# Optimization experiments

Hardware: AMD Instinct MI355X
Metric: run time of the kernel (lower is better)

## Reference

```python
import jax, jax.numpy as jnp
import numpy as np

B, S, D, H, DH = 2, 2048, 1024, 16, 64
R_ATTN, R_OUT, I, R_FC1, R_FC2 = 32, 512, 4096, 512, 512
LN_EPS = 1e-5


def _layernorm(x, g, b):
    mu = jnp.mean(x, axis=-1, keepdims=True)
    var = jnp.mean(jnp.square(x - mu), axis=-1, keepdims=True)
    return (x - mu) * jax.lax.rsqrt(var + LN_EPS) * g + b


def setup_inputs() -> dict:
    key = jax.random.key(0)
    ks = jax.random.split(key, 16)
    std = 0.02
    return {
        'hidden_states': jax.random.normal(ks[0], (B, S, D), jnp.float32),
        'ln1_g': jnp.ones((D,), jnp.float32),
        'ln1_b': jnp.zeros((D,), jnp.float32),
        'ln2_g': jnp.ones((D,), jnp.float32),
        'ln2_b': jnp.zeros((D,), jnp.float32),
        'q_U': jax.random.normal(ks[1], (D, H, R_ATTN), jnp.float32) * std,
        'q_V': jax.random.normal(ks[2], (H, R_ATTN, DH), jnp.float32) * std,
        'q_b': jnp.zeros((H, DH), jnp.float32),
        'k_U': jax.random.normal(ks[3], (D, H, R_ATTN), jnp.float32) * std,
        'k_V': jax.random.normal(ks[4], (H, R_ATTN, DH), jnp.float32) * std,
        'k_b': jnp.zeros((H, DH), jnp.float32),
        'v_U': jax.random.normal(ks[5], (D, H, R_ATTN), jnp.float32) * std,
        'v_V': jax.random.normal(ks[6], (H, R_ATTN, DH), jnp.float32) * std,
        'v_b': jnp.zeros((H, DH), jnp.float32),
        'out_U': jax.random.normal(ks[7], (D, R_OUT), jnp.float32) * std,
        'out_V': jax.random.normal(ks[8], (R_OUT, D), jnp.float32) * std,
        'out_b': jnp.zeros((D,), jnp.float32),
        'fc1_U': jax.random.normal(ks[9], (D, R_FC1), jnp.float32) * std,
        'fc1_V': jax.random.normal(ks[10], (R_FC1, I), jnp.float32) * std,
        'fc1_b': jnp.zeros((I,), jnp.float32),
        'fc2_U': jax.random.normal(ks[11], (I, R_FC2), jnp.float32) * std,
        'fc2_V': jax.random.normal(ks[12], (R_FC2, D), jnp.float32) * std,
        'fc2_b': jnp.zeros((D,), jnp.float32),
    }


def reference(hidden_states, ln1_g, ln1_b, ln2_g, ln2_b,
              q_U, q_V, q_b, k_U, k_V, k_b, v_U, v_V, v_b,
              out_U, out_V, out_b, fc1_U, fc1_V, fc1_b, fc2_U, fc2_V, fc2_b):
    Bx, Sx, Dx = hidden_states.shape
    scale = 1.0 / np.sqrt(DH).astype(np.float32)
    x = _layernorm(hidden_states, ln1_g, ln1_b)
    # low-rank per-head QKV: [B,S,D]x[D,H,r]x[H,r,dh] -> [B,H,S,dh]
    Q = jnp.einsum('bsd,dhr,hre->bhse', x, q_U, q_V) + q_b[None, :, None, :]
    K = jnp.einsum('bsd,dhr,hre->bhse', x, k_U, k_V) + k_b[None, :, None, :]
    V = jnp.einsum('bsd,dhr,hre->bhse', x, v_U, v_V) + v_b[None, :, None, :]
    scores = jnp.einsum('bhse,bhte->bhst', Q, K) * scale  # [B,H,S,S]
    causal = jnp.tril(jnp.ones((Sx, Sx), bool))
    neg_inf = jnp.finfo(scores.dtype).min
    scores = jnp.where(causal, scores, neg_inf)
    probs = jax.nn.softmax(scores, axis=-1)
    Y = jnp.einsum('bhst,bhte->bhse', probs, V)
    Y = Y.transpose(0, 2, 1, 3).reshape(Bx, Sx, Dx)  # merge heads
    Y = (Y @ out_U) @ out_V + out_b
    h = hidden_states + Y
    z = _layernorm(h, ln2_g, ln2_b)
    h1 = jax.nn.gelu((z @ fc1_U) @ fc1_V + fc1_b, approximate=False)
    h2 = (h1 @ fc2_U) @ fc2_V + fc2_b
    return h + h2
```

## Files before the change

### kernel.cpp

```cpp
#include <hip/hip_runtime.h>
#include <cstdint>
#include <cstddef>


#define NTOK 4096
#define DM   1024
#define SEQ  2048

typedef __attribute__((ext_vector_type(8))) __bf16 bf16x8;
typedef __attribute__((ext_vector_type(4))) __bf16 bf16x4;
typedef __attribute__((ext_vector_type(4))) float  f32x4;

__device__ __forceinline__ f32x4 mfma16(bf16x8 a, bf16x8 b, f32x4 c) {
  return __builtin_amdgcn_mfma_f32_16x16x32_bf16(a, b, c, 0, 0, 0);
}

__device__ __forceinline__ void gload16(const __bf16* g, __bf16* l) {
  __builtin_amdgcn_global_load_lds(
      (const __attribute__((address_space(1))) void*)g,
      (__attribute__((address_space(3))) void*)l, 16, 0, 0);
}

__global__ __launch_bounds__(256) void transpose_k(const float* __restrict__ in,
                                                   __bf16* __restrict__ out,
                                                   int R, int C) {
  __shared__ __bf16 t[32][33];
  int tx = threadIdx.x & 31, ty = threadIdx.x >> 5;
  int r0 = blockIdx.y * 32, c0 = blockIdx.x * 32;
#pragma unroll
  for (int i = 0; i < 32; i += 8)
    t[ty + i][tx] = (__bf16)in[(size_t)(r0 + ty + i) * C + c0 + tx];
  __syncthreads();
#pragma unroll
  for (int i = 0; i < 32; i += 8)
    out[(size_t)(c0 + ty + i) * R + r0 + tx] = t[tx][ty + i];
}

__global__ __launch_bounds__(256) void trans_v(const __bf16* __restrict__ qkv,
                                               __bf16* __restrict__ VT) {
  __shared__ __bf16 t[32][33];
  int tx = threadIdx.x & 31, ty = threadIdx.x >> 5;
  int bh = blockIdx.z, b = bh >> 4, h = bh & 15;
  int k0 = blockIdx.x * 32, d0 = blockIdx.y * 32;
#pragma unroll
  for (int i = 0; i < 32; i += 8)
    t[ty + i][tx] = qkv[(size_t)(b * SEQ + k0 + ty + i) * 3072 + 2048 + h * 64 + d0 + tx];
  __syncthreads();
#pragma unroll
  for (int i = 0; i < 32; i += 8)
    VT[(size_t)(bh * 64 + d0 + ty + i) * SEQ + k0 + tx] = t[tx][ty + i];
}

__global__ __launch_bounds__(256) void combine_uv(const float* __restrict__ qU,
                                                  const float* __restrict__ qV,
                                                  const float* __restrict__ kU,
                                                  const float* __restrict__ kV,
                                                  const float* __restrict__ vU,
                                                  const float* __restrict__ vV,
                                                  __bf16* __restrict__ WT) {
  __shared__ float sV[2048];
  int tid = threadIdx.x;
  int blk = blockIdx.x;
  int sel = blk >> 7;
  int rem = blk & 127;
  int h = rem >> 3, dc = rem & 7;
  int d0 = dc << 7;
  const float* U = sel == 0 ? qU : (sel == 1 ? kU : vU);
  const float* V = sel == 0 ? qV : (sel == 1 ? kV : vV);
  for (int i = tid; i < 2048; i += 256) sV[i] = V[h * 2048 + i];
  int d = d0 + (tid & 127);
  int eh = tid >> 7;
  const float* up = U + (size_t)d * 512 + h * 32;
  float u[32];
#pragma unroll
  for (int i = 0; i < 8; i++)
    *(float4*)&u[i * 4] = *(const float4*)(up + i * 4);
  __syncthreads();
  int e0 = eh * 32;
#pragma unroll
  for (int eg = 0; eg < 8; eg++) {
    float ax = 0.f, ay = 0.f, az = 0.f, aw = 0.f;
#pragma unroll
    for (int r = 0; r < 32; r++) {
      float4 v4 = *(const float4*)&sV[r * 64 + e0 + eg * 4];
      ax += u[r] * v4.x; ay += u[r] * v4.y;
      az += u[r] * v4.z; aw += u[r] * v4.w;
    }
    size_t prow = (size_t)(sel * 1024 + h * 64 + e0 + eg * 4) * 1024 + d;
    WT[prow]        = (__bf16)ax;
    WT[prow + 1024] = (__bf16)ay;
    WT[prow + 2048] = (__bf16)az;
    WT[prow + 3072] = (__bf16)aw;
  }
}

__global__ void concat3(const float* a, const float* b, const float* c, float* o) {
  int i = blockIdx.x * 256 + threadIdx.x;
  o[i] = (i < 1024) ? a[i] : (i < 2048 ? b[i - 1024] : c[i - 2048]);
}

__global__ __launch_bounds__(256) void cast_k(const float* __restrict__ in,
                                              __bf16* __restrict__ out, int n) {
  int i = blockIdx.x * 256 + threadIdx.x;
  if (i < n) out[i] = (__bf16)in[i];
}

template <int TWO>
__global__ __launch_bounds__(256) void ln_k(const float* __restrict__ x,
                                            const __bf16* __restrict__ x2,
                                            const float* __restrict__ g,
                                            const float* __restrict__ b,
                                            __bf16* __restrict__ out) {
  int row = blockIdx.x, tid = threadIdx.x;
  const float* xr = x + (size_t)row * DM;
  float v[4], s = 0.f, ss = 0.f;
#pragma unroll
  for (int i = 0; i < 4; i++) {
    int c = i * 256 + tid;
    v[i] = xr[c];
    if (TWO) v[i] += (float)x2[(size_t)row * DM + c];
    s += v[i]; ss += v[i] * v[i];
  }
#pragma unroll
  for (int m = 1; m < 64; m <<= 1) { s += __shfl_xor(s, m); ss += __shfl_xor(ss, m); }
  __shared__ float rs_[4], rss[4];
  if ((tid & 63) == 0) { rs_[tid >> 6] = s; rss[tid >> 6] = ss; }
  __syncthreads();
  s  = rs_[0] + rs_[1] + rs_[2] + rs_[3];
  ss = rss[0] + rss[1] + rss[2] + rss[3];
  float mu  = s * (1.f / 1024.f);
  float var = ss * (1.f / 1024.f) - mu * mu;
  float rstd = rsqrtf(var + 1e-5f);
#pragma unroll
  for (int i = 0; i < 4; i++) {
    int c = i * 256 + tid;
    out[(size_t)row * DM + c] = (__bf16)((v[i] - mu) * rstd * g[c] + b[c]);
  }
}

template <int EPI, int BN>
__global__ __launch_bounds__(256) void gemm_bt(const __bf16* __restrict__ A,
                                               const __bf16* __restrict__ BT,
                                               void* __restrict__ Cv,
                                               const float* __restrict__ bias,
                                               const float* __restrict__ resF,
                                               const __bf16* __restrict__ resB,
                                               int M, int N, int K) {
  constexpr int WR = (BN == 128) ? 4 : 2;
  __shared__ alignas(16) __bf16 la[2][128 * 32];
  __shared__ alignas(16) __bf16 lb[2][BN * 32];
  int tid = threadIdx.x;
  int lane = tid & 63;
  int wave = tid >> 6;
  int quad = lane >> 4, l15 = lane & 15;
  int gx = gridDim.x;
  int nwg = gx * gridDim.y;
  int flat = blockIdx.y * gx + blockIdx.x;
  if ((nwg & 7) == 0) flat = (flat & 7) * (nwg >> 3) + (flat >> 3);
  int bm = (flat / gx) * 128, bn = (flat % gx) * BN;
  int wm = (BN == 128) ? (wave >> 1) * 64 : wave * 32;
  int wn = (BN == 128) ? (wave & 1) * 64 : 0;
  int lr = lane >> 2;
  int lc = (((lane & 3) ^ ((lr >> 1) & 3))) * 8;
  const __bf16* ga = A  + (size_t)(bm + wave * 32 + lr) * K + lc;
  const __bf16* gb = BT + (size_t)(bn + wave * (BN == 128 ? 32 : 16) + lr) * K + lc;
  int ksw = ((l15 >> 1) & 3) * 8;
  f32x4 acc[WR][4] = {};

  auto stage = [&](int k0, int b) {
    __bf16* lab = &la[b][wave * 1024];
    gload16(ga + k0, lab);
    gload16(ga + (size_t)16 * K + k0, lab + 512);
    if (BN == 128) {
      __bf16* lbb = &lb[b][wave * 1024];
      gload16(gb + k0, lbb);
      gload16(gb + (size_t)16 * K + k0, lbb + 512);
    } else {
      gload16(gb + k0, &lb[b][wave * 512]);
    }
  };

  stage(0, 0);
  __syncthreads();
  for (int k0 = 0; k0 < K; k0 += 32) {
    int b = (k0 >> 5) & 1;
    if (k0 + 32 < K) stage(k0 + 32, b ^ 1);
    bf16x8 af[WR], bfr[4];
#pragma unroll
    for (int i = 0; i < WR; i++)
      af[i] = *(const bf16x8*)&la[b][(wm + i * 16 + l15) * 32 + (quad * 8 ^ ksw)];
#pragma unroll
    for (int j = 0; j < 4; j++)
      bfr[j] = *(const bf16x8*)&lb[b][(wn + j * 16 + l15) * 32 + (quad * 8 ^ ksw)];
#pragma unroll
    for (int i = 0; i < WR; i++)
#pragma unroll
      for (int j = 0; j < 4; j++)
        acc[i][j] = mfma16(af[i], bfr[j], acc[i][j]);
    __syncthreads();
  }
#pragma unroll
  for (int i = 0; i < WR; i++) {
#pragma unroll
    for (int j = 0; j < 4; j++) {
      int col = bn + wn + j * 16 + l15;
      float bv = bias ? bias[col] : 0.f;
#pragma unroll
      for (int r = 0; r < 4; r++) {
        int row = bm + wm + i * 16 + quad * 4 + r;
        size_t idx = (size_t)row * N + col;
        float v = acc[i][j][r] + bv;
        if (EPI == 0) {
          ((__bf16*)Cv)[idx] = (__bf16)v;
        } else if (EPI == 1) {
          v = 0.5f * v * (1.f + erff(v * 0.70710678118654752f));
          ((__bf16*)Cv)[idx] = (__bf16)v;
        } else {
          v += resF[idx] + (float)resB[idx];
          ((float*)Cv)[idx] = v;
        }
      }
    }
  }
}

__global__ __launch_bounds__(256) void gemm_bt64s(const __bf16* __restrict__ A,
                                                  const __bf16* __restrict__ BT,
                                                  __bf16* __restrict__ C,
                                                  int M, int N, int K) {
  __shared__ alignas(16) __bf16 la[2][64 * 32];
  __shared__ alignas(16) __bf16 lb[2][64 * 32];
  int tid = threadIdx.x;
  int lane = tid & 63;
  int wave = tid >> 6;
  int quad = lane >> 4, l15 = lane & 15;
  int gx = gridDim.x;
  int nwg = gx * gridDim.y;
  int flat = blockIdx.y * gx + blockIdx.x;
  if ((nwg & 7) == 0) flat = (flat & 7) * (nwg >> 3) + (flat >> 3);
  int bm = (flat / gx) * 64, bn = (flat % gx) * 64;
  int lr = tid >> 2;
  int lc = (((tid & 3) ^ ((lr >> 1) & 3))) * 8;
  const __bf16* ga = A  + (size_t)(bm + lr) * K + lc;
  const __bf16* gb = BT + (size_t)(bn + lr) * K + lc;
  int ksw = ((l15 >> 1) & 3) * 8;
  f32x4 acc[4] = {};

  auto stage = [&](int k0, int b) {
    gload16(ga + k0, &la[b][tid * 8]);
    gload16(gb + k0, &lb[b][tid * 8]);
  };

  stage(0, 0);
  __syncthreads();
  for (int k0 = 0; k0 < K; k0 += 32) {
    int b = (k0 >> 5) & 1;
    if (k0 + 32 < K) stage(k0 + 32, b ^ 1);
    bf16x8 af = *(const bf16x8*)&la[b][(wave * 16 + l15) * 32 + (quad * 8 ^ ksw)];
    bf16x8 bfr[4];
#pragma unroll
    for (int j = 0; j < 4; j++)
      bfr[j] = *(const bf16x8*)&lb[b][(j * 16 + l15) * 32 + (quad * 8 ^ ksw)];
#pragma unroll
    for (int j = 0; j < 4; j++)
      acc[j] = mfma16(af, bfr[j], acc[j]);
    __syncthreads();
  }
#pragma unroll
  for (int j = 0; j < 4; j++) {
    int col = bn + j * 16 + l15;
#pragma unroll
    for (int r = 0; r < 4; r++) {
      int row = bm + wave * 16 + quad * 4 + r;
      C[(size_t)row * N + col] = (__bf16)acc[j][r];
    }
  }
}

__global__ __launch_bounds__(256) void gemm_sk(const __bf16* __restrict__ A,
                                               const __bf16* __restrict__ BT,
                                               float* __restrict__ Cf,
                                               int M, int N, int K, int KS) {
  __shared__ alignas(16) __bf16 la[2][128 * 32];
  __shared__ alignas(16) __bf16 lb[2][128 * 32];
  int tid = threadIdx.x;
  int lane = tid & 63;
  int wave = tid >> 6;
  int quad = lane >> 4, l15 = lane & 15;
  int bm = blockIdx.y * 128, bn = blockIdx.x * 128;
  int wm = (wave >> 1) * 64, wn = (wave & 1) * 64;
  int klen = K / KS;
  int kbeg = blockIdx.z * klen, kend = kbeg + klen;
  int lr = lane >> 2;
  int lc = (((lane & 3) ^ ((lr >> 1) & 3))) * 8;
  const __bf16* ga = A  + (size_t)(bm + wave * 32 + lr) * K + lc;
  const __bf16* gb = BT + (size_t)(bn + wave * 32 + lr) * K + lc;
  int ksw = ((l15 >> 1) & 3) * 8;
  f32x4 acc[4][4] = {};

  auto stage = [&](int k0, int b) {
    __bf16* lab = &la[b][wave * 1024];
    __bf16* lbb = &lb[b][wave * 1024];
    gload16(ga + k0, lab);
    gload16(ga + (size_t)16 * K + k0, lab + 512);
    gload16(gb + k0, lbb);
    gload16(gb + (size_t)16 * K + k0, lbb + 512);
  };

  stage(kbeg, 0);
  __syncthreads();
  for (int k0 = kbeg; k0 < kend; k0 += 32) {
    int b = ((k0 - kbeg) >> 5) & 1;
    if (k0 + 32 < kend) stage(k0 + 32, b ^ 1);
    bf16x8 af[4], bfr[4];
#pragma unroll
    for (int i = 0; i < 4; i++)
      af[i] = *(const bf16x8*)&la[b][(wm + i * 16 + l15) * 32 + (quad * 8 ^ ksw)];
#pragma unroll
    for (int j = 0; j < 4; j++)
      bfr[j] = *(const bf16x8*)&lb[b][(wn + j * 16 + l15) * 32 + (quad * 8 ^ ksw)];
#pragma unroll
    for (int i = 0; i < 4; i++)
#pragma unroll
      for (int j = 0; j < 4; j++)
        acc[i][j] = mfma16(af[i], bfr[j], acc[i][j]);
    __syncthreads();
  }
#pragma unroll
  for (int i = 0; i < 4; i++)
#pragma unroll
    for (int j = 0; j < 4; j++) {
      int col = bn + wn + j * 16 + l15;
#pragma unroll
      for (int r = 0; r < 4; r++) {
        int row = bm + wm + i * 16 + quad * 4 + r;
        atomicAdd(&Cf[(size_t)row * N + col], acc[i][j][r]);
      }
    }
}

#define JOB(q, a, b) ((uint32_t)(q) | ((uint32_t)(a) << 8) | ((uint32_t)(b) << 16))
__device__ const uint32_t JOBTAB[24] = {
  JOB(7, 0, 16),  JOB(15, 0, 16), JOB(15, 16, 32),
  JOB(14, 0, 15), JOB(14, 15, 30),
  JOB(6, 0, 14),  JOB(13, 0, 14), JOB(13, 14, 28),
  JOB(12, 0, 13), JOB(12, 13, 26),
  JOB(5, 0, 12),  JOB(11, 0, 12), JOB(11, 12, 24),
  JOB(10, 0, 11), JOB(10, 11, 22),
  JOB(4, 0, 10),  JOB(9, 0, 10),  JOB(9, 10, 20),
  JOB(8, 0, 9),   JOB(8, 9, 18),
  JOB(3, 0, 8),   JOB(2, 0, 6),   JOB(1, 0, 4),   JOB(0, 0, 2),
};

__global__ __launch_bounds__(512, 6) void attn_k(const __bf16* __restrict__ QKV,
                                                 const __bf16* __restrict__ VT,
                                                 __bf16* __restrict__ Y,
                                                 float* __restrict__ Opart,
                                                 float* __restrict__ lpart) {
  const float SC = 0.18033688011112042f;
  const float C2 = 23.083120654223414f;
  __shared__ alignas(16) __bf16 lk[2][64 * 64];
  __shared__ alignas(16) __bf16 lv[2][64 * 64];
  __shared__ alignas(16) __bf16 P[8][16 * 72];
  int tid = threadIdx.x;
  int wave = tid >> 6, lane = tid & 63;
  int quad = lane >> 4, l15 = lane & 15;
  int bh = blockIdx.x & 31;
  int job = blockIdx.x >> 5;
  uint32_t jt = JOBTAB[job];
  int qb = jt & 255, kbeg = (jt >> 8) & 255, kend = (jt >> 16) & 255;
  bool split = qb >= 8;
  int b = bh >> 4, h = bh & 15;
  int q0w = (qb << 7) + wave * 16;
  const size_t RS = 3 * DM;
  const __bf16* base = QKV + (size_t)b * SEQ * RS;
  const __bf16* vtb  = VT + (size_t)bh * 64 * SEQ;

  const __bf16* qp = base + (size_t)(q0w + l15) * RS + h * 64 + quad * 8;
  bf16x8 aq0 = *(const bf16x8*)qp;
  bf16x8 aq1 = *(const bf16x8*)(qp + 32);

  int srow = tid >> 3, schunk = tid & 7;
  int sswz = (schunk ^ (srow & 7)) << 3;
  const __bf16* gk_src = base + (size_t)srow * RS + DM + h * 64 + sswz;
  const __bf16* gv_src = vtb + (size_t)srow * SEQ + sswz;

  int c0 = (quad ^ (l15 & 7)) << 3;
  int c1 = ((quad + 4) ^ (l15 & 7)) << 3;

  f32x4 zero4 = {0.f, 0.f, 0.f, 0.f};
  f32x4 O[4] = {zero4, zero4, zero4, zero4};
  float l_i = 0.f;

  int ntiles = kend - kbeg;

  gload16(gk_src + ((size_t)kbeg << 6) * RS, &lk[0][tid * 8]);
  gload16(gv_src + ((size_t)kbeg << 6),      &lv[0][tid * 8]);
  __syncthreads();

  for (int t = 0; t < ntiles; t++) {
    int kt = kbeg + t;
    int cur = t & 1;
    if (t + 1 < ntiles) {
      size_t kn = (size_t)(kt + 1) << 6;
      gload16(gk_src + kn * RS, &lk[cur ^ 1][tid * 8]);
      gload16(gv_src + kn,      &lv[cur ^ 1][tid * 8]);
    }
    int k0 = kt << 6;
    if (k0 <= q0w + 15) {
      f32x4 s[4] = {zero4, zero4, zero4, zero4};
#pragma unroll
      for (int gk = 0; gk < 4; gk++) {
        const __bf16* kr = &lk[cur][(gk * 16 + l15) * 64];
        bf16x8 kb0 = *(const bf16x8*)(kr + c0);
        bf16x8 kb1 = *(const bf16x8*)(kr + c1);
        s[gk] = mfma16(kb0, aq0, s[gk]);
        s[gk] = mfma16(kb1, aq1, s[gk]);
      }
      if (k0 + 63 <= q0w) {
#pragma unroll
        for (int gk = 0; gk < 4; gk++) {
          float p0 = exp2f(fmaf(s[gk][0], SC, -C2));
          float p1 = exp2f(fmaf(s[gk][1], SC, -C2));
          float p2 = exp2f(fmaf(s[gk][2], SC, -C2));
          float p3 = exp2f(fmaf(s[gk][3], SC, -C2));
          l_i += (p0 + p1) + (p2 + p3);
          bf16x4 pw = {(__bf16)p0, (__bf16)p1, (__bf16)p2, (__bf16)p3};
          *(bf16x4*)&P[wave][l15 * 72 + gk * 16 + quad * 4] = pw;
        }
      } else {
        int qrow = q0w + l15;
#pragma unroll
        for (int gk = 0; gk < 4; gk++) {
          int kb = k0 + gk * 16 + quad * 4;
          float p0 = (kb     <= qrow) ? exp2f(fmaf(s[gk][0], SC, -C2)) : 0.f;
          float p1 = (kb + 1 <= qrow) ? exp2f(fmaf(s[gk][1], SC, -C2)) : 0.f;
          float p2 = (kb + 2 <= qrow) ? exp2f(fmaf(s[gk][2], SC, -C2)) : 0.f;
          float p3 = (kb + 3 <= qrow) ? exp2f(fmaf(s[gk][3], SC, -C2)) : 0.f;
          l_i += (p0 + p1) + (p2 + p3);
          bf16x4 pw = {(__bf16)p0, (__bf16)p1, (__bf16)p2, (__bf16)p3};
          *(bf16x4*)&P[wave][l15 * 72 + gk * 16 + quad * 4] = pw;
        }
      }
      bf16x8 ap0 = *(const bf16x8*)&P[wave][l15 * 72 + quad * 8];
      bf16x8 ap1 = *(const bf16x8*)&P[wave][l15 * 72 + 32 + quad * 8];
#pragma unroll
      for (int nt = 0; nt < 4; nt++) {
        const __bf16* vr = &lv[cur][(nt * 16 + l15) * 64];
        bf16x8 bv0 = *(const bf16x8*)(vr + c0);
        bf16x8 bv1 = *(const bf16x8*)(vr + c1);
        O[nt] = mfma16(ap0, bv0, O[nt]);
        O[nt] = mfma16(ap1, bv1, O[nt]);
      }
    }
    __syncthreads();
  }

  l_i += __shfl_xor(l_i, 16);
  l_i += __shfl_xor(l_i, 32);
  if (!split) {
#pragma unroll
    for (int r = 0; r < 4; r++) {
      float inv = 1.f / __shfl(l_i, quad * 4 + r);
      size_t orow = (size_t)(b * SEQ + q0w + quad * 4 + r);
      __bf16* yp = Y + orow * DM + h * 64 + l15;
      yp[0]  = (__bf16)(O[0][r] * inv);
      yp[16] = (__bf16)(O[1][r] * inv);
      yp[32] = (__bf16)(O[2][r] * inv);
      yp[48] = (__bf16)(O[3][r] * inv);
    }
  } else {
#pragma unroll
    for (int r = 0; r < 4; r++) {
      int row = (q0w - 1024) + quad * 4 + r;
      float* op = Opart + (((size_t)bh << 10) + row) * 64 + l15;
      atomicAdd(op +  0, O[0][r]);
      atomicAdd(op + 16, O[1][r]);
      atomicAdd(op + 32, O[2][r]);
      atomicAdd(op + 48, O[3][r]);
    }
    if (quad == 0)
      atomicAdd(&lpart[((size_t)bh << 10) + (q0w - 1024) + l15], l_i);
  }
}

__global__ __launch_bounds__(256) void norm_k(const float* __restrict__ Op,
                                              const float* __restrict__ lp,
                                              __bf16* __restrict__ Y) {
  int idx = blockIdx.x * 256 + threadIdx.x;
  int dh = idx & 63;
  int row = (idx >> 6) & 1023;
  int bh = idx >> 16;
  int b = bh >> 4, h = bh & 15;
  float inv = 1.f / lp[(bh << 10) + row];
  Y[(size_t)(b * SEQ + 1024 + row) * DM + h * 64 + dh] = (__bf16)(Op[idx] * inv);
}

extern "C" void kernel_launch(void* const* d_in, const int* in_sizes, int n_in,
                              void* d_out, int out_size, void* d_ws, size_t ws_size,
                              hipStream_t stream) {
  (void)in_sizes; (void)n_in; (void)out_size; (void)ws_size;
  const float* hidden = (const float*)d_in[0];
  const float* ln1_g  = (const float*)d_in[1];
  const float* ln1_b  = (const float*)d_in[2];
  const float* ln2_g  = (const float*)d_in[3];
  const float* ln2_b  = (const float*)d_in[4];
  const float* q_U = (const float*)d_in[5];
  const float* q_V = (const float*)d_in[6];
  const float* q_b = (const float*)d_in[7];
  const float* k_U = (const float*)d_in[8];
  const float* k_V = (const float*)d_in[9];
  const float* k_b = (const float*)d_in[10];
  const float* v_U = (const float*)d_in[11];
  const float* v_V = (const float*)d_in[12];
  const float* v_b = (const float*)d_in[13];
  const float* out_U = (const float*)d_in[14];
  const float* out_V = (const float*)d_in[15];
  const float* out_b = (const float*)d_in[16];
  const float* fc1_U = (const float*)d_in[17];
  const float* fc1_V = (const float*)d_in[18];
  const float* fc1_b = (const float*)d_in[19];
  const float* fc2_U = (const float*)d_in[20];
  const float* fc2_V = (const float*)d_in[21];
  const float* fc2_b = (const float*)d_in[22];

  const size_t MB = 1u << 20;
  char* ws = (char*)d_ws;
  __bf16* outUT = (__bf16*)(ws + 0 * MB);
  __bf16* outVT = (__bf16*)(ws + 1 * MB);
  __bf16* f1UT  = (__bf16*)(ws + 2 * MB);
  __bf16* f1VT  = (__bf16*)(ws + 3 * MB);
  __bf16* f2VT  = (__bf16*)(ws + 7 * MB);
  float*  bqkv  = (float*) (ws + 8 * MB);
  __bf16* wqkvT = (__bf16*)(ws + 9 * MB);
  __bf16* f2UT  = (__bf16*)(ws + 9 * MB);
  __bf16* xln   = (__bf16*)(ws + 15 * MB);
  __bf16* yattn = (__bf16*)(ws + 15 * MB);
  __bf16* zbuf  = (__bf16*)(ws + 15 * MB);
  float*  t3f32 = (float*) (ws + 15 * MB);
  __bf16* t3bf  = (__bf16*)(ws + 19 * MB);
  __bf16* qkv   = (__bf16*)(ws + 23 * MB);
  __bf16* h1c   = (__bf16*)(ws + 23 * MB);
  __bf16* tbuf  = (__bf16*)(ws + 43 * MB);
  __bf16* VT    = (__bf16*)(ws + 47 * MB);
  __bf16* hres  = (__bf16*)(ws + 47 * MB);
  float* Opart = (float*)d_out;
  float* lpart = (float*)d_out + 2097152;

  transpose_k<<<dim3(16, 32), 256, 0, stream>>>(out_U, outUT, 1024, 512);
  transpose_k<<<dim3(32, 16), 256, 0, stream>>>(out_V, outVT, 512, 1024);
  transpose_k<<<dim3(16, 32), 256, 0, stream>>>(fc1_U, f1UT, 1024, 512);
  transpose_k<<<dim3(128, 16), 256, 0, stream>>>(fc1_V, f1VT, 512, 4096);
  transpose_k<<<dim3(32, 16), 256, 0, stream>>>(fc2_V, f2VT, 512, 1024);
  combine_uv<<<384, 256, 0, stream>>>(q_U, q_V, k_U, k_V, v_U, v_V, wqkvT);
  concat3<<<12, 256, 0, stream>>>(q_b, k_b, v_b, bqkv);

  ln_k<0><<<NTOK, 256, 0, stream>>>(hidden, nullptr, ln1_g, ln1_b, xln);
  gemm_bt<0, 128><<<dim3(24, 32), 256, 0, stream>>>(xln, wqkvT, qkv, bqkv,
                                                    nullptr, nullptr, NTOK, 3072, 1024);
  transpose_k<<<dim3(16, 128), 256, 0, stream>>>(fc2_U, f2UT, 4096, 512);
  trans_v<<<dim3(64, 2, 32), 256, 0, stream>>>(qkv, VT);
  hipMemsetAsync(d_out, 0, (size_t)8519680, stream);
  attn_k<<<768, 512, 0, stream>>>(qkv, VT, yattn, Opart, lpart);
  norm_k<<<8192, 256, 0, stream>>>(Opart, lpart, yattn);
  gemm_bt64s<<<dim3(8, 64), 256, 0, stream>>>(yattn, outUT, tbuf, NTOK, 512, 1024);
  gemm_bt<0, 64><<<dim3(16, 32), 256, 0, stream>>>(tbuf, outVT, hres, out_b,
                                                   nullptr, nullptr, NTOK, 1024, 512);
  ln_k<1><<<NTOK, 256, 0, stream>>>(hidden, hres, ln2_g, ln2_b, zbuf);
  gemm_bt64s<<<dim3(8, 64), 256, 0, stream>>>(zbuf, f1UT, tbuf, NTOK, 512, 1024);
  for (int mc = 0; mc < 2; mc++) {
    __bf16* tchunk = tbuf + (size_t)mc * 2048 * 512;
    gemm_bt<1, 128><<<dim3(32, 16), 256, 0, stream>>>(tchunk, f1VT, h1c, fc1_b,
                                                      nullptr, nullptr, 2048, 4096, 512);
    hipMemsetAsync(t3f32, 0, (size_t)2048 * 512 * 4, stream);
    gemm_sk<<<dim3(4, 16, 4), 256, 0, stream>>>(h1c, f2UT, t3f32,
                                                2048, 512, 4096, 4);
    cast_k<<<4096, 256, 0, stream>>>(t3f32, t3bf + (size_t)mc * 2048 * 512,
                                     2048 * 512);
  }
  gemm_bt<3, 64><<<dim3(16, 32), 256, 0, stream>>>(t3bf, f2VT, (float*)d_out, fc2_b,
                                                   hidden, hres, NTOK, 1024, 512);
}
```

Before: 423.4 us.

## Fuse weight prep kernels, unchunk FC1/FC2, split-K partial buffers, tanh GELU

```diff
diff --git a/kernel.cpp b/kernel.cpp
--- a/kernel.cpp
+++ b/kernel.cpp
@@ -34,6 +34,42 @@
 #pragma unroll
   for (int i = 0; i < 32; i += 8)
     out[(size_t)(c0 + ty + i) * R + r0 + tx] = t[tx][ty + i];
+}
+
+__global__ __launch_bounds__(256) void prep_k(
+    const float* __restrict__ qb, const float* __restrict__ kb,
+    const float* __restrict__ vb, float* __restrict__ bqkv,
+    const float* __restrict__ outU, __bf16* __restrict__ outUT,
+    const float* __restrict__ outV, __bf16* __restrict__ outVT,
+    const float* __restrict__ f1U,  __bf16* __restrict__ f1UT,
+    const float* __restrict__ f1V,  __bf16* __restrict__ f1VT,
+    const float* __restrict__ f2V,  __bf16* __restrict__ f2VT,
+    const float* __restrict__ f2U,  __bf16* __restrict__ f2UT) {
+  int blk = blockIdx.x;
+  if (blk < 12) {
+    int i = blk * 256 + threadIdx.x;
+    bqkv[i] = (i < 1024) ? qb[i] : (i < 2048 ? kb[i - 1024] : vb[i - 2048]);
+    return;
+  }
+  int t = blk - 12;
+  const float* in; __bf16* out; int R, C;
+  if (t < 512)       { in = outU; out = outUT; R = 1024; C = 512;  }
+  else if (t < 1024) { in = outV; out = outVT; R = 512;  C = 1024; t -= 512; }
+  else if (t < 1536) { in = f1U;  out = f1UT;  R = 1024; C = 512;  t -= 1024; }
+  else if (t < 3584) { in = f1V;  out = f1VT;  R = 512;  C = 4096; t -= 1536; }
+  else if (t < 4096) { in = f2V;  out = f2VT;  R = 512;  C = 1024; t -= 3584; }
+  else               { in = f2U;  out = f2UT;  R = 4096; C = 512;  t -= 4096; }
+  int ct = C >> 5;
+  int c0 = (t % ct) * 32, r0 = (t / ct) * 32;
+  __shared__ __bf16 tt[32][33];
+  int tx = threadIdx.x & 31, ty = threadIdx.x >> 5;
+#pragma unroll
+  for (int i = 0; i < 32; i += 8)
+    tt[ty + i][tx] = (__bf16)in[(size_t)(r0 + ty + i) * C + c0 + tx];
+  __syncthreads();
+#pragma unroll
+  for (int i = 0; i < 32; i += 8)
+    out[(size_t)(c0 + ty + i) * R + r0 + tx] = tt[tx][ty + i];
 }
 
 __global__ __launch_bounds__(256) void trans_v(const __bf16* __restrict__ qkv,
@@ -94,15 +130,17 @@
   }
 }
 
-__global__ void concat3(const float* a, const float* b, const float* c, float* o) {
-  int i = blockIdx.x * 256 + threadIdx.x;
-  o[i] = (i < 1024) ? a[i] : (i < 2048 ? b[i - 1024] : c[i - 2048]);
-}
-
 __global__ __launch_bounds__(256) void cast_k(const float* __restrict__ in,
                                               __bf16* __restrict__ out, int n) {
   int i = blockIdx.x * 256 + threadIdx.x;
   if (i < n) out[i] = (__bf16)in[i];
+}
+
+__global__ __launch_bounds__(256) void merge4_k(const float* __restrict__ p,
+                                                __bf16* __restrict__ out) {
+  int i = blockIdx.x * 256 + threadIdx.x;
+  float s = (p[i] + p[i + 2097152]) + (p[i + 4194304] + p[i + 6291456]);
+  out[i] = (__bf16)s;
 }
 
 template <int TWO>
@@ -213,7 +251,10 @@
         if (EPI == 0) {
           ((__bf16*)Cv)[idx] = (__bf16)v;
         } else if (EPI == 1) {
-          v = 0.5f * v * (1.f + erff(v * 0.70710678118654752f));
+          float y = 0.79788456080286536f * fmaf(0.044715f * v, v * v, v);
+          float u = exp2f(y * 2.885390081777926f);
+          float th = (u - 1.f) / (u + 1.f);
+          v = 0.5f * v * (1.f + th);
           ((__bf16*)Cv)[idx] = (__bf16)v;
         } else {
           v += resF[idx] + (float)resB[idx];
@@ -277,6 +318,7 @@
   }
 }
 
+template <int ATOMIC>
 __global__ __launch_bounds__(256) void gemm_sk(const __bf16* __restrict__ A,
                                                const __bf16* __restrict__ BT,
                                                float* __restrict__ Cf,
@@ -326,6 +368,7 @@
         acc[i][j] = mfma16(af[i], bfr[j], acc[i][j]);
     __syncthreads();
   }
+  float* out = ATOMIC ? Cf : Cf + (size_t)blockIdx.z * M * N;
 #pragma unroll
   for (int i = 0; i < 4; i++)
 #pragma unroll
@@ -334,7 +377,8 @@
 #pragma unroll
       for (int r = 0; r < 4; r++) {
         int row = bm + wm + i * 16 + quad * 4 + r;
-        atomicAdd(&Cf[(size_t)row * N + col], acc[i][j][r]);
+        if (ATOMIC) atomicAdd(&out[(size_t)row * N + col], acc[i][j][r]);
+        else        out[(size_t)row * N + col] = acc[i][j][r];
       }
     }
 }
@@ -499,7 +543,7 @@
 extern "C" void kernel_launch(void* const* d_in, const int* in_sizes, int n_in,
                               void* d_out, int out_size, void* d_ws, size_t ws_size,
                               hipStream_t stream) {
-  (void)in_sizes; (void)n_in; (void)out_size; (void)ws_size;
+  (void)in_sizes; (void)n_in; (void)out_size;
   const float* hidden = (const float*)d_in[0];
   const float* ln1_g  = (const float*)d_in[1];
   const float* ln1_b  = (const float*)d_in[2];
@@ -526,6 +570,7 @@
 
   const size_t MB = 1u << 20;
   char* ws = (char*)d_ws;
+  bool big = ws_size >= 112 * MB;
   __bf16* outUT = (__bf16*)(ws + 0 * MB);
   __bf16* outVT = (__bf16*)(ws + 1 * MB);
   __bf16* f1UT  = (__bf16*)(ws + 2 * MB);
@@ -533,32 +578,33 @@
   __bf16* f2VT  = (__bf16*)(ws + 7 * MB);
   float*  bqkv  = (float*) (ws + 8 * MB);
   __bf16* wqkvT = (__bf16*)(ws + 9 * MB);
-  __bf16* f2UT  = (__bf16*)(ws + 9 * MB);
+  __bf16* f2UT  = big ? (__bf16*)(ws + 55 * MB)
+                      : (__bf16*)(ws + 9 * MB);
   __bf16* xln   = (__bf16*)(ws + 15 * MB);
   __bf16* yattn = (__bf16*)(ws + 15 * MB);
   __bf16* zbuf  = (__bf16*)(ws + 15 * MB);
   float*  t3f32 = (float*) (ws + 15 * MB);
   __bf16* t3bf  = (__bf16*)(ws + 19 * MB);
   __bf16* qkv   = (__bf16*)(ws + 23 * MB);
-  __bf16* h1c   = (__bf16*)(ws + 23 * MB);
+  __bf16* h1c   = big ? (__bf16*)(ws + 64 * MB)
+                      : (__bf16*)(ws + 23 * MB);
+  float*  t3p   = (float*) (ws + 96 * MB);
   __bf16* tbuf  = (__bf16*)(ws + 43 * MB);
   __bf16* VT    = (__bf16*)(ws + 47 * MB);
   __bf16* hres  = (__bf16*)(ws + 47 * MB);
   float* Opart = (float*)d_out;
   float* lpart = (float*)d_out + 2097152;
 
-  transpose_k<<<dim3(16, 32), 256, 0, stream>>>(out_U, outUT, 1024, 512);
-  transpose_k<<<dim3(32, 16), 256, 0, stream>>>(out_V, outVT, 512, 1024);
-  transpose_k<<<dim3(16, 32), 256, 0, stream>>>(fc1_U, f1UT, 1024, 512);
-  transpose_k<<<dim3(128, 16), 256, 0, stream>>>(fc1_V, f1VT, 512, 4096);
-  transpose_k<<<dim3(32, 16), 256, 0, stream>>>(fc2_V, f2VT, 512, 1024);
+  prep_k<<<big ? 6156 : 4108, 256, 0, stream>>>(
+      q_b, k_b, v_b, bqkv, out_U, outUT, out_V, outVT,
+      fc1_U, f1UT, fc1_V, f1VT, fc2_V, f2VT, fc2_U, f2UT);
   combine_uv<<<384, 256, 0, stream>>>(q_U, q_V, k_U, k_V, v_U, v_V, wqkvT);
-  concat3<<<12, 256, 0, stream>>>(q_b, k_b, v_b, bqkv);
 
   ln_k<0><<<NTOK, 256, 0, stream>>>(hidden, nullptr, ln1_g, ln1_b, xln);
   gemm_bt<0, 128><<<dim3(24, 32), 256, 0, stream>>>(xln, wqkvT, qkv, bqkv,
                                                     nullptr, nullptr, NTOK, 3072, 1024);
-  transpose_k<<<dim3(16, 128), 256, 0, stream>>>(fc2_U, f2UT, 4096, 512);
+  if (!big)
+    transpose_k<<<dim3(16, 128), 256, 0, stream>>>(fc2_U, f2UT, 4096, 512);
   trans_v<<<dim3(64, 2, 32), 256, 0, stream>>>(qkv, VT);
   hipMemsetAsync(d_out, 0, (size_t)8519680, stream);
   attn_k<<<768, 512, 0, stream>>>(qkv, VT, yattn, Opart, lpart);
@@ -568,15 +614,23 @@
                                                    nullptr, nullptr, NTOK, 1024, 512);
   ln_k<1><<<NTOK, 256, 0, stream>>>(hidden, hres, ln2_g, ln2_b, zbuf);
   gemm_bt64s<<<dim3(8, 64), 256, 0, stream>>>(zbuf, f1UT, tbuf, NTOK, 512, 1024);
-  for (int mc = 0; mc < 2; mc++) {
-    __bf16* tchunk = tbuf + (size_t)mc * 2048 * 512;
-    gemm_bt<1, 128><<<dim3(32, 16), 256, 0, stream>>>(tchunk, f1VT, h1c, fc1_b,
-                                                      nullptr, nullptr, 2048, 4096, 512);
-    hipMemsetAsync(t3f32, 0, (size_t)2048 * 512 * 4, stream);
-    gemm_sk<<<dim3(4, 16, 4), 256, 0, stream>>>(h1c, f2UT, t3f32,
-                                                2048, 512, 4096, 4);
-    cast_k<<<4096, 256, 0, stream>>>(t3f32, t3bf + (size_t)mc * 2048 * 512,
-                                     2048 * 512);
+  if (big) {
+    gemm_bt<1, 128><<<dim3(32, 32), 256, 0, stream>>>(tbuf, f1VT, h1c, fc1_b,
+                                                      nullptr, nullptr, NTOK, 4096, 512);
+    gemm_sk<0><<<dim3(4, 32, 4), 256, 0, stream>>>(h1c, f2UT, t3p,
+                                                   NTOK, 512, 4096, 4);
+    merge4_k<<<8192, 256, 0, stream>>>(t3p, t3bf);
+  } else {
+    for (int mc = 0; mc < 2; mc++) {
+      __bf16* tchunk = tbuf + (size_t)mc * 2048 * 512;
+      gemm_bt<1, 128><<<dim3(32, 16), 256, 0, stream>>>(tchunk, f1VT, h1c, fc1_b,
+                                                        nullptr, nullptr, 2048, 4096, 512);
+      hipMemsetAsync(t3f32, 0, (size_t)2048 * 512 * 4, stream);
+      gemm_sk<1><<<dim3(4, 16, 4), 256, 0, stream>>>(h1c, f2UT, t3f32,
+                                                     2048, 512, 4096, 4);
+      cast_k<<<4096, 256, 0, stream>>>(t3f32, t3bf + (size_t)mc * 2048 * 512,
+                                       2048 * 512);
+    }
   }
   gemm_bt<3, 64><<<dim3(16, 32), 256, 0, stream>>>(t3bf, f2VT, (float*)d_out, fc2_b,
                                                    hidden, hres, NTOK, 1024, 512);
```

Measured after the change: 369.0 us. 1.15x faster.
